# Kernel optimization log

Measured on AMD Instinct MI355X. Metric: run time of the kernel, lower is better.

The kernel has to match this reference:

```python
import jax, jax.numpy as jnp
import numpy as np

B, S, NH, HID, NL = 64, 512, 16, 512, 16
W_WIN, PAD, THR, BW = 5, 2, 5.0, 0.1
D_IN = 1 + 2 * NH


def setup_inputs():
    key = jax.random.key(0)
    ks = jax.random.split(key, 16)
    time = jax.random.uniform(ks[0], (B, S)) * 1000.0
    mag = 15.0 + jax.random.normal(ks[1], (B, S))
    err = 0.01 + 0.1 * jax.random.uniform(ks[2], (B, S))
    sc = 0.05
    p = {}
    p["light_curve"] = jnp.stack([time, mag, err], axis=1)  # (B,3,S)
    p["valid_mask"] = jnp.ones((B, S), dtype=bool)
    p["frequency"] = 0.5 + 4.5 * jax.random.uniform(ks[3], (B,))
    p["W_ih0"] = sc * jax.random.normal(ks[4], (3 * HID, D_IN))
    p["b_ih0"] = jnp.zeros((3 * HID,))
    p["W_hh0"] = sc * jax.random.normal(ks[5], (3 * HID, HID))
    p["b_hh0"] = jnp.zeros((3 * HID,))
    p["W_ih1"] = sc * jax.random.normal(ks[6], (3 * HID, HID))
    p["b_ih1"] = jnp.zeros((3 * HID,))
    p["W_hh1"] = sc * jax.random.normal(ks[7], (3 * HID, HID))
    p["b_hh1"] = jnp.zeros((3 * HID,))
    p["Wl1"] = sc * jax.random.normal(ks[8], (HID, HID))
    p["bl1"] = jnp.zeros((HID,))
    p["Wl2"] = sc * jax.random.normal(ks[9], (NL, HID))
    p["bl2"] = jnp.zeros((NL,))
    return p


def _flag_outliers(phase, mag):
    # Sorted-window weighted (Epanechnikov in circular phase-delta) mean/std outlier test.
    # Caller guarantees all points valid (setup uses an all-True mask), so index_select == identity.
    perm = jnp.argsort(phase)
    ps, ms = phase[perm], mag[perm]

    def windows(x):
        xp = jnp.concatenate([x[-PAD:], x, x[:PAD]])  # circular pad
        return jnp.stack([xp[i:i + S] for i in range(W_WIN)], axis=-1)  # (S, w)

    wp, wm = windows(ps), windows(ms)
    cols = jnp.array([i for i in range(W_WIN) if i != PAD])
    dphi = wp[:, cols] - wp[:, PAD:PAD + 1]
    dphi = jnp.remainder(dphi - 0.5, 1.0) - 0.5
    wgt = 0.75 * (1.0 - dphi ** 2)
    wmm = wm[:, cols]
    wsum = wgt.sum(-1)
    loc = (wmm * wgt).sum(-1) / wsum
    scale = jnp.sqrt((((wmm - loc[:, None]) ** 2) * wgt).sum(-1) / (wsum - 1.0))
    thr = loc + THR * scale
    sigma = jnp.zeros_like(mag).at[perm].set(thr)  # inverse-permute (index_copy_)
    return mag > sigma


def _gru_layer(x, W_ih, b_ih, W_hh, b_hh):
    # torch nn.GRU cell math; x: (B,S,D) -> (B,S,H)
    xW = jnp.einsum('bsd,gd->bsg', x, W_ih) + b_ih  # (B,S,3H)

    def step(h, xt):
        hW = h @ W_hh.T + b_hh
        xr, xz, xn = jnp.split(xt, 3, axis=-1)
        hr, hz, hn = jnp.split(hW, 3, axis=-1)
        r = jax.nn.sigmoid(xr + hr)
        z = jax.nn.sigmoid(xz + hz)
        n = jnp.tanh(xn + r * hn)
        h = (1.0 - z) * n + z * h
        return h, h

    h0 = jnp.zeros((x.shape[0], W_hh.shape[1]), x.dtype)
    _, hs = jax.lax.scan(step, h0, jnp.swapaxes(xW, 0, 1))
    return jnp.swapaxes(hs, 0, 1)


def reference(light_curve, valid_mask, frequency, W_ih0, b_ih0, W_hh0, b_hh0,
              W_ih1, b_ih1, W_hh1, b_hh1, Wl1, bl1, Wl2, bl2):
    time, mag, err = light_curve[:, 0], light_curve[:, 1], light_curve[:, 2]
    period = 2.0 / frequency[:, None]  # fold_with_double_period=True (default)
    phase = jnp.remainder(time, period) / period
    outlier = jax.vmap(_flag_outliers)(phase, mag)
    is_valid = valid_mask & ~outlier

    # periodic-kernel interpolation on 50-point grid; align phase to brightness max
    grid = jnp.linspace(0.0, 1.0, 50)
    delta = grid[None, :, None] - phase[:, None, :]  # (B,50,S)
    K = jnp.exp((jnp.cos(2.0 * jnp.pi * delta) - 1.0) / BW ** 2)
    Wk = is_valid[:, None, :].astype(K.dtype) * K
    Wk = Wk / Wk.sum(-1, keepdims=True)
    smooth = (Wk * mag[:, None, :]).sum(-1)  # (B,50)
    phase = phase - grid[jnp.argmax(smooth, axis=-1)][:, None]

    # sort by phase, invalid points last; scaler=None -> loc 0, scale 1
    big = jnp.finfo(jnp.float32).max
    idx = jnp.argsort(jnp.where(is_valid, phase, big), axis=-1)
    phase = jnp.take_along_axis(phase, idx, -1)
    mag = jnp.take_along_axis(mag, idx, -1)
    is_valid = jnp.take_along_axis(is_valid, idx, -1)

    # Fourier phase embedding [cos_1..cos_H, sin_1..sin_H] + mag -> (B,S,2H+1)
    k = jnp.arange(1, NH + 1, dtype=phase.dtype)
    ang = 2.0 * jnp.pi * phase[:, :, None] * k
    emb = jnp.concatenate([jnp.cos(ang), jnp.sin(ang), mag[:, :, None]], axis=-1)

    ht = _gru_layer(emb, W_ih0, b_ih0, W_hh0, b_hh0)
    ht = _gru_layer(ht, W_ih1, b_ih1, W_hh1, b_hh1)

    m = is_valid[:, :, None].astype(ht.dtype)  # context='average'
    ctx = (ht * m).sum(1) / m.sum(1)
    h1 = jax.nn.gelu(ctx @ Wl1.T + bl1, approximate=False)
    z = h1 @ Wl2.T + bl2
    return z
```

## Files before the change

kernel.cpp:

```cpp
#include <hip/hip_runtime.h>


typedef unsigned short u16;
typedef unsigned int u32;
typedef unsigned long long u64;

__device__ __forceinline__ float b2f(u16 u) { return __uint_as_float(((u32)u) << 16); }
__device__ __forceinline__ float blo(u32 u) { return __uint_as_float(u << 16); }
__device__ __forceinline__ float bhi(u32 u) { return __uint_as_float(u & 0xffff0000u); }
__device__ __forceinline__ u16 f2b(float f) {
    u32 x = __float_as_uint(f);
    u32 r = x + 0x7fffu + ((x >> 16) & 1u);
    return (u16)(r >> 16);
}

#define SS 512
#define TWO_PI 6.28318530717958647692f
#define BIGF 3.402823466e+38f
#define PANEL_ELEMS (1536 * 512)
#define FLAGS_BYTES 32768
#define FL(g, f) (((g) * 16 + (f)) * 16)
#define F_A 0
#define F_B 2
#define F_C 4
#define G_A 6
#define G_B 8
#define G_C 10
#define F_PRE 12
#define F_CTX 14

struct P {
    const void* lc;
    const void* freq;
    const void* W[12];
    void* out;
    void* ws;
    unsigned long long ws_size;
};

__device__ __forceinline__ bool inputs_are_bf16(const void* freq) {
    const u16* q = (const u16*)freq;
    bool ok = true;
    for (int i = 0; i < 64; ++i) {
        float v = b2f(q[i]);
        ok = ok && (v >= 0.4f) && (v <= 5.5f);
    }
    return ok;
}

template<bool BF>
__device__ __forceinline__ float ldw(const void* p, size_t i) {
    if constexpr (BF) return b2f(((const u16*)p)[i]);
    else              return ((const float*)p)[i];
}
template<bool BF>
__device__ __forceinline__ const void* rowp(const void* base, int row) {
    if constexpr (BF) return (const void*)((const u16*)base + (size_t)row * 512);
    else              return (const void*)((const float*)base + (size_t)row * 512);
}

__device__ __forceinline__ void sc_store_f(float* ptr, float v) {
    __hip_atomic_store(ptr, v, __ATOMIC_RELAXED, __HIP_MEMORY_SCOPE_AGENT);
}
__device__ __forceinline__ float sc_load_f(const float* ptr) {
    return __hip_atomic_load(ptr, __ATOMIC_RELAXED, __HIP_MEMORY_SCOPE_AGENT);
}
__device__ __forceinline__ void sc_store_i(int* ptr, int v) {
    __hip_atomic_store(ptr, v, __ATOMIC_RELAXED, __HIP_MEMORY_SCOPE_AGENT);
}
__device__ __forceinline__ int sc_load_i(const int* ptr) {
    return __hip_atomic_load(ptr, __ATOMIC_RELAXED, __HIP_MEMORY_SCOPE_AGENT);
}
__device__ __forceinline__ void waitge(const int* f, int v, int* dead) {
    if (*dead) return;
    int it = 0;
    while (sc_load_i(f) < v) {
        __builtin_amdgcn_s_sleep(1);
        if (++it > 400000) { *dead = 1; break; }
    }
}

template<bool BF>
__device__ void build_panel_one(const void* W, int tid, char* panbase) {
    if constexpr (BF) {
        const uint4* Ws = (const uint4*)W;
        uint4* panel = (uint4*)panbase;
        for (int i = tid; i < 1536 * 64; i += 512) {
            int r = i >> 6, k8 = i & 63;
            panel[(size_t)k8 * 1536 + r] = Ws[i];
        }
    } else {
        const float4* Ws = (const float4*)W;
        float4* panel = (float4*)panbase;
        for (int i = tid; i < 1536 * 128; i += 512) {
            int r = i >> 7, k4 = i & 127;
            panel[(size_t)k4 * 1536 + r] = Ws[i];
        }
    }
}
template<bool BF>
__device__ void build_piece(const void* W, int half, int tid, char* panbase) {
    if constexpr (BF) {
        const uint4* Ws = (const uint4*)W;
        uint4* panel = (uint4*)panbase;
        for (int i = tid; i < 768 * 64; i += 512) {
            int r768 = i >> 6, k8 = i & 63;
            int g3 = r768 >> 8, r = r768 & 255;
            int srcrow = g3 * 512 + half * 256 + r;
            panel[(size_t)k8 * 768 + r768] = Ws[(size_t)srcrow * 64 + k8];
        }
    } else {
        const float4* Ws = (const float4*)W;
        float4* panel = (float4*)panbase;
        for (int i = tid; i < 768 * 128; i += 512) {
            int r768 = i >> 7, k4 = i & 127;
            int g3 = r768 >> 8, r = r768 & 255;
            int srcrow = g3 * 512 + half * 256 + r;
            panel[(size_t)k4 * 768 + r768] = Ws[(size_t)srcrow * 128 + k4];
        }
    }
}

template<bool BF>
__device__ __forceinline__ void tridot_panel(const void* panel, int j,
                                             const float* __restrict__ sh,
                                             float& ar, float& az, float& an) {
    if constexpr (BF) {
        const uint4* pr = (const uint4*)panel + j;
        const uint4* pz = pr + 512;
        const uint4* pn = pr + 1024;
        for (int k0 = 0; k0 < 512; k0 += 8) {
            size_t o = (size_t)(k0 >> 3) * 1536;
            float4 h0 = *(const float4*)&sh[k0];
            float4 h1 = *(const float4*)&sh[k0 + 4];
            uint4 a = pr[o], c = pz[o], d = pn[o];
            ar += blo(a.x) * h0.x + bhi(a.x) * h0.y + blo(a.y) * h0.z + bhi(a.y) * h0.w
                + blo(a.z) * h1.x + bhi(a.z) * h1.y + blo(a.w) * h1.z + bhi(a.w) * h1.w;
            az += blo(c.x) * h0.x + bhi(c.x) * h0.y + blo(c.y) * h0.z + bhi(c.y) * h0.w
                + blo(c.z) * h1.x + bhi(c.z) * h1.y + blo(c.w) * h1.z + bhi(c.w) * h1.w;
            an += blo(d.x) * h0.x + bhi(d.x) * h0.y + blo(d.y) * h0.z + bhi(d.y) * h0.w
                + blo(d.z) * h1.x + bhi(d.z) * h1.y + blo(d.w) * h1.z + bhi(d.w) * h1.w;
        }
    } else {
        const float4* pr = (const float4*)panel + j;
        const float4* pz = pr + 512;
        const float4* pn = pr + 1024;
        for (int k0 = 0; k0 < 512; k0 += 8) {
            size_t o = (size_t)(k0 >> 2) * 1536;
            float4 h0 = *(const float4*)&sh[k0];
            float4 h1 = *(const float4*)&sh[k0 + 4];
            float4 a0 = pr[o], a1 = pr[o + 1536];
            float4 c0 = pz[o], c1 = pz[o + 1536];
            float4 d0 = pn[o], d1 = pn[o + 1536];
            ar += a0.x * h0.x + a0.y * h0.y + a0.z * h0.z + a0.w * h0.w
                + a1.x * h1.x + a1.y * h1.y + a1.z * h1.z + a1.w * h1.w;
            az += c0.x * h0.x + c0.y * h0.y + c0.z * h0.z + c0.w * h0.w
                + c1.x * h1.x + c1.y * h1.y + c1.z * h1.z + c1.w * h1.w;
            an += d0.x * h0.x + d0.y * h0.y + d0.z * h0.z + d0.w * h0.w
                + d1.x * h1.x + d1.y * h1.y + d1.z * h1.z + d1.w * h1.w;
        }
    }
}

template<bool BF>
__device__ __forceinline__ void tridot2(const void* panel, int r, int kh,
                                        const float* __restrict__ ha,
                                        const float* __restrict__ hb,
                                        float& a0r, float& a0z, float& a0n,
                                        float& a1r, float& a1z, float& a1n) {
    const int kbeg = kh * 256;
    if constexpr (BF) {
        const uint4* pr = (const uint4*)panel + r;
        const uint4* pz = pr + 256;
        const uint4* pn = pr + 512;
        for (int k0 = kbeg; k0 < kbeg + 256; k0 += 8) {
            size_t o = (size_t)(k0 >> 3) * 768;
            float4 ha0 = *(const float4*)&ha[k0];
            float4 ha1 = *(const float4*)&ha[k0 + 4];
            float4 hb0 = *(const float4*)&hb[k0];
            float4 hb1 = *(const float4*)&hb[k0 + 4];
            uint4 a = pr[o], c = pz[o], d = pn[o];
            a0r += blo(a.x)*ha0.x + bhi(a.x)*ha0.y + blo(a.y)*ha0.z + bhi(a.y)*ha0.w
                 + blo(a.z)*ha1.x + bhi(a.z)*ha1.y + blo(a.w)*ha1.z + bhi(a.w)*ha1.w;
            a1r += blo(a.x)*hb0.x + bhi(a.x)*hb0.y + blo(a.y)*hb0.z + bhi(a.y)*hb0.w
                 + blo(a.z)*hb1.x + bhi(a.z)*hb1.y + blo(a.w)*hb1.z + bhi(a.w)*hb1.w;
            a0z += blo(c.x)*ha0.x + bhi(c.x)*ha0.y + blo(c.y)*ha0.z + bhi(c.y)*ha0.w
                 + blo(c.z)*ha1.x + bhi(c.z)*ha1.y + blo(c.w)*ha1.z + bhi(c.w)*ha1.w;
            a1z += blo(c.x)*hb0.x + bhi(c.x)*hb0.y + blo(c.y)*hb0.z + bhi(c.y)*hb0.w
                 + blo(c.z)*hb1.x + bhi(c.z)*hb1.y + blo(c.w)*hb1.z + bhi(c.w)*hb1.w;
            a0n += blo(d.x)*ha0.x + bhi(d.x)*ha0.y + blo(d.y)*ha0.z + bhi(d.y)*ha0.w
                 + blo(d.z)*ha1.x + bhi(d.z)*ha1.y + blo(d.w)*ha1.z + bhi(d.w)*ha1.w;
            a1n += blo(d.x)*hb0.x + bhi(d.x)*hb0.y + blo(d.y)*hb0.z + bhi(d.y)*hb0.w
                 + blo(d.z)*hb1.x + bhi(d.z)*hb1.y + blo(d.w)*hb1.z + bhi(d.w)*hb1.w;
        }
    } else {
        const float4* pr = (const float4*)panel + r;
        const float4* pz = pr + 256;
        const float4* pn = pr + 512;
        for (int k0 = kbeg; k0 < kbeg + 256; k0 += 8) {
            size_t o = (size_t)(k0 >> 2) * 768;
            float4 ha0 = *(const float4*)&ha[k0];
            float4 ha1 = *(const float4*)&ha[k0 + 4];
            float4 hb0 = *(const float4*)&hb[k0];
            float4 hb1 = *(const float4*)&hb[k0 + 4];
            float4 a0 = pr[o], a1 = pr[o + 768];
            float4 c0 = pz[o], c1 = pz[o + 768];
            float4 d0 = pn[o], d1 = pn[o + 768];
            a0r += a0.x*ha0.x + a0.y*ha0.y + a0.z*ha0.z + a0.w*ha0.w
                 + a1.x*ha1.x + a1.y*ha1.y + a1.z*ha1.z + a1.w*ha1.w;
            a1r += a0.x*hb0.x + a0.y*hb0.y + a0.z*hb0.z + a0.w*hb0.w
                 + a1.x*hb1.x + a1.y*hb1.y + a1.z*hb1.z + a1.w*hb1.w;
            a0z += c0.x*ha0.x + c0.y*ha0.y + c0.z*ha0.z + c0.w*ha0.w
                 + c1.x*ha1.x + c1.y*ha1.y + c1.z*ha1.z + c1.w*ha1.w;
            a1z += c0.x*hb0.x + c0.y*hb0.y + c0.z*hb0.z + c0.w*hb0.w
                 + c1.x*hb1.x + c1.y*hb1.y + c1.z*hb1.z + c1.w*hb1.w;
            a0n += d0.x*ha0.x + d0.y*ha0.y + d0.z*ha0.z + d0.w*ha0.w
                 + d1.x*ha1.x + d1.y*ha1.y + d1.z*ha1.z + d1.w*ha1.w;
            a1n += d0.x*hb0.x + d0.y*hb0.y + d0.z*hb0.z + d0.w*hb0.w
                 + d1.x*hb1.x + d1.y*hb1.y + d1.z*hb1.z + d1.w*hb1.w;
        }
    }
}

template<bool BF>
__device__ __forceinline__ float dot512(const void* vr, const float* __restrict__ sh) {
    float acc = 0.f;
    if constexpr (BF) {
        const u32* pr = (const u32*)vr;
        for (int k0 = 0; k0 < 512; k0 += 8) {
            float4 h0 = *(const float4*)&sh[k0];
            float4 h1 = *(const float4*)&sh[k0 + 4];
            uint4 a = *(const uint4*)(pr + (k0 >> 1));
            acc += blo(a.x) * h0.x + bhi(a.x) * h0.y + blo(a.y) * h0.z + bhi(a.y) * h0.w
                 + blo(a.z) * h1.x + bhi(a.z) * h1.y + blo(a.w) * h1.z + bhi(a.w) * h1.w;
        }
    } else {
        const float* pr = (const float*)vr;
        for (int k0 = 0; k0 < 512; k0 += 8) {
            float4 h0 = *(const float4*)&sh[k0];
            float4 h1 = *(const float4*)&sh[k0 + 4];
            float4 a0 = *(const float4*)(pr + k0), a1 = *(const float4*)(pr + k0 + 4);
            acc += a0.x * h0.x + a0.y * h0.y + a0.z * h0.z + a0.w * h0.w
                 + a1.x * h1.x + a1.y * h1.y + a1.z * h1.z + a1.w * h1.w;
        }
    }
    return acc;
}

struct PreShm {
    float ph[512], mg[512], skey[512], sig[512], vld[512];
    int   sidx[512];
    float ps2[512], ms2[512], vs2[512];
    float pn[50][8], pd[50][8], smoothv[50];
    float gshift, nv;
};

__device__ void bitonic512(float* skey, int* sidx, int tid) {
    for (int k = 2; k <= 512; k <<= 1) {
        for (int j = k >> 1; j > 0; j >>= 1) {
            int ixj = tid ^ j;
            if (ixj > tid) {
                float ka = skey[tid], kb = skey[ixj];
                int ia = sidx[tid], ib = sidx[ixj];
                bool up = ((tid & k) == 0);
                bool agtb = (ka > kb) || (ka == kb && ia > ib);
                if (agtb == up) {
                    skey[tid] = kb; skey[ixj] = ka;
                    sidx[tid] = ib; sidx[ixj] = ia;
                }
            }
            __syncthreads();
        }
    }
}

template<bool BF>
__device__ void preproc_core(const P& p, PreShm& s, int b, int tid) {
    float period = 2.0f / ldw<BF>(p.freq, b);
    float t = ldw<BF>(p.lc, (size_t)b * 3 * SS + tid);
    float m = ldw<BF>(p.lc, (size_t)b * 3 * SS + SS + tid);
    float ph0 = fmodf(t, period) / period;
    s.ph[tid] = ph0; s.mg[tid] = m;
    s.skey[tid] = ph0; s.sidx[tid] = tid;
    __syncthreads();
    bitonic512(s.skey, s.sidx, tid);
    {
        float pc = s.skey[tid];
        float wv[4], mv[4];
        float wsum = 0.f, wm = 0.f;
        const int offs[4] = {-2, -1, 1, 2};
#pragma unroll
        for (int c = 0; c < 4; ++c) {
            int jj = (tid + offs[c]) & 511;
            float d = s.skey[jj] - pc;
            float u = d - 0.5f; u = u - floorf(u);
            float dphi = u - 0.5f;
            float w = 0.75f * (1.0f - dphi * dphi);
            float mm = s.mg[s.sidx[jj]];
            wv[c] = w; mv[c] = mm;
            wsum += w; wm += w * mm;
        }
        float loc = wm / wsum;
        float s2 = 0.f;
#pragma unroll
        for (int c = 0; c < 4; ++c) { float dm = mv[c] - loc; s2 += dm * dm * wv[c]; }
        float scale = sqrtf(s2 / (wsum - 1.0f));
        s.sig[s.sidx[tid]] = loc + 5.0f * scale;
    }
    __syncthreads();
    s.vld[tid] = (s.mg[tid] > s.sig[tid]) ? 0.0f : 1.0f;
    __syncthreads();
    if (tid == 0) {
        float acc = 0.f;
        for (int i = 0; i < 512; ++i) acc += s.vld[i];
        s.nv = acc;
    }
    {
        int g = tid >> 3, pq = tid & 7;
        if (g < 50) {
            float gv = (float)g * (1.0f / 49.0f);
            float num = 0.f, den = 0.f;
            int s0 = pq * 64;
            for (int ss = s0; ss < s0 + 64; ++ss) {
                float d = gv - s.ph[ss];
                float c = cosf(TWO_PI * d);
                float K = expf((c - 1.0f) * 100.0f);
                float w = s.vld[ss] * K;
                den += w; num += w * s.mg[ss];
            }
            s.pn[g][pq] = num; s.pd[g][pq] = den;
        }
    }
    __syncthreads();
    if (tid < 50) {
        float num = 0.f, den = 0.f;
#pragma unroll
        for (int c = 0; c < 8; ++c) { num += s.pn[tid][c]; den += s.pd[tid][c]; }
        s.smoothv[tid] = num / den;
    }
    __syncthreads();
    if (tid == 0) {
        float best = s.smoothv[0]; int bi = 0;
        for (int g = 1; g < 50; ++g) if (s.smoothv[g] > best) { best = s.smoothv[g]; bi = g; }
        s.gshift = (float)bi * (1.0f / 49.0f);
    }
    __syncthreads();
    float p2 = s.ph[tid] - s.gshift;
    s.ph[tid] = p2;
    s.skey[tid] = (s.vld[tid] > 0.f) ? p2 : BIGF;
    s.sidx[tid] = tid;
    __syncthreads();
    bitonic512(s.skey, s.sidx, tid);
    {
        int o = s.sidx[tid];
        s.ps2[tid] = s.ph[o]; s.ms2[tid] = s.mg[o]; s.vs2[tid] = s.vld[o];
    }
    __syncthreads();
}

struct ShmA {
    PreShm pre;
    float psb[2][512], msb[2][512];
    float h0L[1024];
    float eL[2][34];
    float part[6][256];
    float xp[3][256];
};
struct ShmB { float h0loc[1024]; float part[6][256]; };
struct ShmC {
    float h1L[1024]; float vs2L[2][512]; float nvL[2];
    float ctxL[512], gL[512]; float part[6][256];
};
struct ShmOldA { PreShm pre; float h0[512], h1[512], eL[34]; };
struct ShmU {
    union { ShmA a; ShmB b; ShmC c; ShmOldA o; } u;
    int dead;
};

template<bool BF, bool PAN>
__device__ void run_all(const P& p, ShmU& S) {
    PreShm& pre = S.u.o.pre;
    float* h0 = S.u.o.h0;
    float* h1 = S.u.o.h1;
    float* eL = S.u.o.eL;
    int b = blockIdx.x, tid = threadIdx.x;
    char* panbase = (char*)p.ws + FLAGS_BYTES;
    const size_t PMAT = (size_t)PANEL_ELEMS * (BF ? 2 : 4);

    if constexpr (PAN) {
        build_panel_one<BF>(p.W[2], tid, panbase);
        build_panel_one<BF>(p.W[4], tid, panbase + PMAT);
        build_panel_one<BF>(p.W[6], tid, panbase + 2 * PMAT);
        __threadfence();
    }
    preproc_core<BF>(p, pre, b, tid);

    int j = tid;
    float wr0[33], wz0[33], wn0[33];
#pragma unroll
    for (int d = 0; d < 33; ++d) {
        wr0[d] = ldw<BF>(p.W[0], (size_t)j * 33 + d);
        wz0[d] = ldw<BF>(p.W[0], ((size_t)j + 512) * 33 + d);
        wn0[d] = ldw<BF>(p.W[0], ((size_t)j + 1024) * 33 + d);
    }
    float bi0r = ldw<BF>(p.W[1], j), bi0z = ldw<BF>(p.W[1], j + 512), bi0n = ldw<BF>(p.W[1], j + 1024);
    float bh0r = ldw<BF>(p.W[3], j), bh0z = ldw<BF>(p.W[3], j + 512), bh0n = ldw<BF>(p.W[3], j + 1024);
    float bi1r = ldw<BF>(p.W[5], j), bi1z = ldw<BF>(p.W[5], j + 512), bi1n = ldw<BF>(p.W[5], j + 1024);
    float bh1r = ldw<BF>(p.W[7], j), bh1z = ldw<BF>(p.W[7], j + 512), bh1n = ldw<BF>(p.W[7], j + 1024);

    const void* pan0  = (const void*)panbase;
    const void* pan1x = (const void*)(panbase + PMAT);
    const void* pan1h = (const void*)(panbase + 2 * PMAT);
    const void *w0r = rowp<BF>(p.W[2], j), *w0z = rowp<BF>(p.W[2], j + 512), *w0n = rowp<BF>(p.W[2], j + 1024);
    const void *x1r = rowp<BF>(p.W[4], j), *x1z = rowp<BF>(p.W[4], j + 512), *x1n = rowp<BF>(p.W[4], j + 1024);
    const void *w1r = rowp<BF>(p.W[6], j), *w1z = rowp<BF>(p.W[6], j + 512), *w1n = rowp<BF>(p.W[6], j + 1024);

    h0[j] = 0.f; h1[j] = 0.f;
    float cacc = 0.f;
    __syncthreads();

    for (int tt = 0; tt < 512; ++tt) {
        if (j < 16) {
            float ang = TWO_PI * pre.ps2[tt] * (float)(j + 1);
            float sv, cv; sincosf(ang, &sv, &cv);
            eL[j] = cv; eL[16 + j] = sv;
        }
        if (j == 32) eL[32] = pre.ms2[tt];
        __syncthreads();
        float xr = bi0r, xz = bi0z, xn = bi0n;
#pragma unroll
        for (int d = 0; d < 33; ++d) {
            float e = eL[d];
            xr += wr0[d] * e; xz += wz0[d] * e; xn += wn0[d] * e;
        }
        float ar = bh0r, az = bh0z, an = bh0n;
        if constexpr (PAN) tridot_panel<BF>(pan0, j, h0, ar, az, an);
        else {
            for (int k = 0; k < 512; ++k) {
                float h = h0[k];
                ar += ldw<BF>(w0r, k) * h; az += ldw<BF>(w0z, k) * h; an += ldw<BF>(w0n, k) * h;
            }
        }
        float h0prev = h0[j];
        float r0 = 1.0f / (1.0f + expf(-(xr + ar)));
        float z0 = 1.0f / (1.0f + expf(-(xz + az)));
        float n0 = tanhf(xn + r0 * an);
        float nh0 = (1.0f - z0) * n0 + z0 * h0prev;
        __syncthreads();
        h0[j] = nh0;
        __syncthreads();
        float yr = bi1r, yz = bi1z, yn = bi1n;
        float cr = bh1r, cz = bh1z, cn = bh1n;
        if constexpr (PAN) {
            tridot_panel<BF>(pan1x, j, h0, yr, yz, yn);
            tridot_panel<BF>(pan1h, j, h1, cr, cz, cn);
        } else {
            for (int k = 0; k < 512; ++k) {
                float h = h0[k], g = h1[k];
                yr += ldw<BF>(x1r, k) * h; yz += ldw<BF>(x1z, k) * h; yn += ldw<BF>(x1n, k) * h;
                cr += ldw<BF>(w1r, k) * g; cz += ldw<BF>(w1z, k) * g; cn += ldw<BF>(w1n, k) * g;
            }
        }
        float h1prev = h1[j];
        float r1 = 1.0f / (1.0f + expf(-(yr + cr)));
        float z1 = 1.0f / (1.0f + expf(-(yz + cz)));
        float n1 = tanhf(yn + r1 * cn);
        float nh1 = (1.0f - z1) * n1 + z1 * h1prev;
        cacc += pre.vs2[tt] * nh1;
        __syncthreads();
        h1[j] = nh1;
    }
    __syncthreads();

    h0[j] = cacc / pre.nv;
    __syncthreads();
    float a1 = ldw<BF>(p.W[9], j) + dot512<BF>(rowp<BF>(p.W[8], j), h0);
    float g = 0.5f * a1 * (1.0f + erff(a1 * 0.70710678118654752440f));
    __syncthreads();
    h1[j] = g;
    __syncthreads();
    if (j < 16) {
        float a2 = ldw<BF>(p.W[11], j) + dot512<BF>(rowp<BF>(p.W[10], j), h1);
        if constexpr (BF) ((u16*)p.out)[(size_t)b * 16 + j] = f2b(a2);
        else              ((float*)p.out)[(size_t)b * 16 + j] = a2;
    }
}

__global__ __launch_bounds__(512) void fused_kernel_old(P p) {
    __shared__ ShmU S;
    bool bf = inputs_are_bf16(p.freq);
    u64 PMAT = bf ? 1572864ull : 3145728ull;
    bool pan = (p.ws && p.ws_size >= (u64)FLAGS_BYTES + 3 * PMAT);
    if (bf) { if (pan) run_all<true, true>(p, S);  else run_all<true, false>(p, S); }
    else    { if (pan) run_all<false, true>(p, S); else run_all<false, false>(p, S); }
}


template<bool BF>
__device__ void runA(const P& p, ShmU& S, int g, int hf, int tid, char* pan,
                     float* h0r, float* pp, int* flags) {
    int* dead = &S.dead;
    build_piece<BF>(p.W[2], hf, tid, pan);
    __threadfence();
    int myb = 2 * g + hf, ob = 2 * g + (1 - hf);
    preproc_core<BF>(p, S.u.a.pre, myb, tid);
    sc_store_f(&pp[(size_t)myb * 2048 + tid], S.u.a.pre.ps2[tid]);
    sc_store_f(&pp[(size_t)myb * 2048 + 512 + tid], S.u.a.pre.ms2[tid]);
    sc_store_f(&pp[(size_t)myb * 2048 + 1024 + tid], S.u.a.pre.vs2[tid]);
    if (tid == 0) sc_store_f(&pp[(size_t)myb * 2048 + 1536], S.u.a.pre.nv);
    asm volatile("s_waitcnt vmcnt(0)" ::: "memory");
    __syncthreads();
    if (tid == 0) sc_store_i(&flags[FL(g, F_PRE + hf)], 1);
    S.u.a.psb[hf][tid] = S.u.a.pre.ps2[tid];
    S.u.a.msb[hf][tid] = S.u.a.pre.ms2[tid];
    if (tid == 0) waitge(&flags[FL(g, F_PRE + (1 - hf))], 1, dead);
    __syncthreads();
    S.u.a.psb[1 - hf][tid] = sc_load_f(&pp[(size_t)ob * 2048 + tid]);
    S.u.a.msb[1 - hf][tid] = sc_load_f(&pp[(size_t)ob * 2048 + 512 + tid]);

    const int r = tid & 255, kh = tid >> 8;
    const int j = hf * 256 + r;
    const float bi0r = ldw<BF>(p.W[1], j), bi0z = ldw<BF>(p.W[1], j + 512), bi0n = ldw<BF>(p.W[1], j + 1024);
    const float bh0r = ldw<BF>(p.W[3], j), bh0z = ldw<BF>(p.W[3], j + 512), bh0n = ldw<BF>(p.W[3], j + 1024);

    float* h0L = S.u.a.h0L;
    h0L[tid] = 0.f; h0L[tid + 512] = 0.f;
    __syncthreads();

    for (int t = 0; t < 512; ++t) {
        if (t > 0) {
            if (tid == 0) waitge(&flags[FL(g, F_A + (1 - hf))], t, dead);
            __syncthreads();
            h0L[kh * 512 + (1 - hf) * 256 + r] =
                sc_load_f(&h0r[(size_t)g * 2048 + ((t - 1) & 1) * 1024 + (1 - hf) * 512 + kh * 256 + r]);
            __syncthreads();
            if (tid == 0) sc_store_i(&flags[FL(g, G_A + hf)], t);
        }
        if (tid < 16) {
            float ang = TWO_PI * S.u.a.psb[0][t] * (float)(tid + 1);
            float sv, cv; sincosf(ang, &sv, &cv);
            S.u.a.eL[0][tid] = cv; S.u.a.eL[0][16 + tid] = sv;
        } else if (tid < 32) {
            int k = tid - 16;
            float ang = TWO_PI * S.u.a.psb[1][t] * (float)(k + 1);
            float sv, cv; sincosf(ang, &sv, &cv);
            S.u.a.eL[1][k] = cv; S.u.a.eL[1][16 + k] = sv;
        }
        if (tid == 32) S.u.a.eL[0][32] = S.u.a.msb[0][t];
        if (tid == 33) S.u.a.eL[1][32] = S.u.a.msb[1][t];
        __syncthreads();

        float xr = bi0r, xz = bi0z, xn = bi0n;
#pragma unroll
        for (int d = 0; d < 33; ++d) {
            float e = S.u.a.eL[kh][d];
            xr += ldw<BF>(p.W[0], (size_t)j * 33 + d) * e;
            xz += ldw<BF>(p.W[0], ((size_t)j + 512) * 33 + d) * e;
            xn += ldw<BF>(p.W[0], ((size_t)j + 1024) * 33 + d) * e;
        }
        float p0r = 0.f, p0z = 0.f, p0n = 0.f, p1r = 0.f, p1z = 0.f, p1n = 0.f;
        tridot2<BF>(pan, r, kh, &h0L[0], &h0L[512], p0r, p0z, p0n, p1r, p1z, p1n);
        if (kh == 1) {
            S.u.a.part[0][r] = p0r; S.u.a.part[1][r] = p0z; S.u.a.part[2][r] = p0n;
            S.u.a.part[3][r] = p1r; S.u.a.part[4][r] = p1z; S.u.a.part[5][r] = p1n;
            S.u.a.xp[0][r] = xr; S.u.a.xp[1][r] = xz; S.u.a.xp[2][r] = xn;
        }
        __syncthreads();
        float nh00 = 0.f, nh01 = 0.f;
        if (kh == 0) {
            float ar0 = bh0r + p0r + S.u.a.part[0][r];
            float az0 = bh0z + p0z + S.u.a.part[1][r];
            float an0 = bh0n + p0n + S.u.a.part[2][r];
            float ar1 = bh0r + p1r + S.u.a.part[3][r];
            float az1 = bh0z + p1z + S.u.a.part[4][r];
            float an1 = bh0n + p1n + S.u.a.part[5][r];
            float x1r = S.u.a.xp[0][r], x1z = S.u.a.xp[1][r], x1n = S.u.a.xp[2][r];
            float h0p0 = h0L[j], h0p1 = h0L[512 + j];
            float r0 = 1.f / (1.f + expf(-(xr + ar0)));
            float z0 = 1.f / (1.f + expf(-(xz + az0)));
            float n0 = tanhf(xn + r0 * an0);
            nh00 = (1.f - z0) * n0 + z0 * h0p0;
            float r1 = 1.f / (1.f + expf(-(x1r + ar1)));
            float z1 = 1.f / (1.f + expf(-(x1z + az1)));
            float n1 = tanhf(x1n + r1 * an1);
            nh01 = (1.f - z1) * n1 + z1 * h0p1;
            h0L[j] = nh00; h0L[512 + j] = nh01;
        }
        if (t >= 2) {
            if (tid == 0) waitge(&flags[FL(g, G_A + (1 - hf))], t - 1, dead);
            if (tid == 1) waitge(&flags[FL(g, G_B + 0)], t - 1, dead);
            if (tid == 2) waitge(&flags[FL(g, G_B + 1)], t - 1, dead);
        }
        __syncthreads();
        if (kh == 0) {
            float* dst = &h0r[(size_t)g * 2048 + (t & 1) * 1024 + hf * 512];
            sc_store_f(&dst[r], nh00);
            sc_store_f(&dst[256 + r], nh01);
        }
        asm volatile("s_waitcnt vmcnt(0)" ::: "memory");
        __syncthreads();
        if (tid == 0) sc_store_i(&flags[FL(g, F_A + hf)], t + 1);
    }
}

template<bool BF>
__device__ void runB(const P& p, ShmU& S, int g, int hf, int tid, char* pan,
                     float* h0r, float* yrng, int* flags) {
    int* dead = &S.dead;
    build_piece<BF>(p.W[4], hf, tid, pan);
    __threadfence();
    __syncthreads();
    const int r = tid & 255, kh = tid >> 8;
    const int j = hf * 256 + r;
    const float bi1r = ldw<BF>(p.W[5], j), bi1z = ldw<BF>(p.W[5], j + 512), bi1n = ldw<BF>(p.W[5], j + 1024);
    float* h0loc = S.u.b.h0loc;

    for (int t = 0; t < 512; ++t) {
        if (tid == 0) waitge(&flags[FL(g, F_A + 0)], t + 1, dead);
        if (tid == 1) waitge(&flags[FL(g, F_A + 1)], t + 1, dead);
        __syncthreads();
        const float* src = &h0r[(size_t)g * 2048 + (t & 1) * 1024];
        h0loc[kh * 512 + r]       = sc_load_f(&src[0 * 512 + kh * 256 + r]);
        h0loc[kh * 512 + 256 + r] = sc_load_f(&src[1 * 512 + kh * 256 + r]);
        __syncthreads();
        if (tid == 0) sc_store_i(&flags[FL(g, G_B + hf)], t + 1);
        float p0r = 0.f, p0z = 0.f, p0n = 0.f, p1r = 0.f, p1z = 0.f, p1n = 0.f;
        tridot2<BF>(pan, r, kh, &h0loc[0], &h0loc[512], p0r, p0z, p0n, p1r, p1z, p1n);
        if (kh == 1) {
            S.u.b.part[0][r] = p0r; S.u.b.part[1][r] = p0z; S.u.b.part[2][r] = p0n;
            S.u.b.part[3][r] = p1r; S.u.b.part[4][r] = p1z; S.u.b.part[5][r] = p1n;
        }
        if (tid == 0 && t >= 2) waitge(&flags[FL(g, G_C + hf)], t - 1, dead);
        __syncthreads();
        if (kh == 0) {
            float y0r = bi1r + p0r + S.u.b.part[0][r];
            float y0z = bi1z + p0z + S.u.b.part[1][r];
            float y0n = bi1n + p0n + S.u.b.part[2][r];
            float y1r = bi1r + p1r + S.u.b.part[3][r];
            float y1z = bi1z + p1z + S.u.b.part[4][r];
            float y1n = bi1n + p1n + S.u.b.part[5][r];
            float* slot = &yrng[(size_t)g * 6144 + (t & 1) * 3072 + hf * 1536];
            sc_store_f(&slot[r], y0r);         sc_store_f(&slot[256 + r], y1r);
            sc_store_f(&slot[512 + r], y0z);   sc_store_f(&slot[768 + r], y1z);
            sc_store_f(&slot[1024 + r], y0n);  sc_store_f(&slot[1280 + r], y1n);
        }
        asm volatile("s_waitcnt vmcnt(0)" ::: "memory");
        __syncthreads();
        if (tid == 0) sc_store_i(&flags[FL(g, F_B + hf)], t + 1);
    }
}

template<bool BF>
__device__ void runC(const P& p, ShmU& S, int g, int hf, int tid, char* pan,
                     float* yrng, float* h1r, float* pp, float* ctxb, int* flags) {
    int* dead = &S.dead;
    build_piece<BF>(p.W[6], hf, tid, pan);
    __threadfence();
    if (tid == 0) waitge(&flags[FL(g, F_PRE + 0)], 1, dead);
    if (tid == 1) waitge(&flags[FL(g, F_PRE + 1)], 1, dead);
    __syncthreads();
    S.u.c.vs2L[0][tid] = sc_load_f(&pp[(size_t)(2 * g) * 2048 + 1024 + tid]);
    S.u.c.vs2L[1][tid] = sc_load_f(&pp[(size_t)(2 * g + 1) * 2048 + 1024 + tid]);
    if (tid == 0) {
        S.u.c.nvL[0] = sc_load_f(&pp[(size_t)(2 * g) * 2048 + 1536]);
        S.u.c.nvL[1] = sc_load_f(&pp[(size_t)(2 * g + 1) * 2048 + 1536]);
    }
    float* h1L = S.u.c.h1L;
    h1L[tid] = 0.f; h1L[tid + 512] = 0.f;
    __syncthreads();

    const int r = tid & 255, kh = tid >> 8;
    const int j = hf * 256 + r;
    const float bh1r = ldw<BF>(p.W[7], j), bh1z = ldw<BF>(p.W[7], j + 512), bh1n = ldw<BF>(p.W[7], j + 1024);
    float cacc0 = 0.f, cacc1 = 0.f;

    for (int t = 0; t < 512; ++t) {
        if (tid == 0) waitge(&flags[FL(g, F_B + hf)], t + 1, dead);
        if (t > 0 && tid == 1) waitge(&flags[FL(g, F_C + (1 - hf))], t, dead);
        __syncthreads();
        if (t > 0) {
            h1L[kh * 512 + (1 - hf) * 256 + r] =
                sc_load_f(&h1r[(size_t)g * 2048 + ((t - 1) & 1) * 1024 + (1 - hf) * 512 + kh * 256 + r]);
        }
        float y0r = 0.f, y0z = 0.f, y0n = 0.f, y1r = 0.f, y1z = 0.f, y1n = 0.f;
        if (kh == 0) {
            const float* slot = &yrng[(size_t)g * 6144 + (t & 1) * 3072 + hf * 1536];
            y0r = sc_load_f(&slot[r]);         y1r = sc_load_f(&slot[256 + r]);
            y0z = sc_load_f(&slot[512 + r]);   y1z = sc_load_f(&slot[768 + r]);
            y0n = sc_load_f(&slot[1024 + r]);  y1n = sc_load_f(&slot[1280 + r]);
        }
        __syncthreads();
        if (tid == 0) sc_store_i(&flags[FL(g, G_C + hf)], t + 1);
        float p0r = 0.f, p0z = 0.f, p0n = 0.f, p1r = 0.f, p1z = 0.f, p1n = 0.f;
        tridot2<BF>(pan, r, kh, &h1L[0], &h1L[512], p0r, p0z, p0n, p1r, p1z, p1n);
        if (kh == 1) {
            S.u.c.part[0][r] = p0r; S.u.c.part[1][r] = p0z; S.u.c.part[2][r] = p0n;
            S.u.c.part[3][r] = p1r; S.u.c.part[4][r] = p1z; S.u.c.part[5][r] = p1n;
        }
        __syncthreads();
        float nh10 = 0.f, nh11 = 0.f;
        if (kh == 0) {
            float cr0 = bh1r + p0r + S.u.c.part[0][r];
            float cz0 = bh1z + p0z + S.u.c.part[1][r];
            float cn0 = bh1n + p0n + S.u.c.part[2][r];
            float cr1 = bh1r + p1r + S.u.c.part[3][r];
            float cz1 = bh1z + p1z + S.u.c.part[4][r];
            float cn1 = bh1n + p1n + S.u.c.part[5][r];
            float h1p0 = h1L[j], h1p1 = h1L[512 + j];
            float r0 = 1.f / (1.f + expf(-(y0r + cr0)));
            float z0 = 1.f / (1.f + expf(-(y0z + cz0)));
            float n0 = tanhf(y0n + r0 * cn0);
            nh10 = (1.f - z0) * n0 + z0 * h1p0;
            float r1 = 1.f / (1.f + expf(-(y1r + cr1)));
            float z1 = 1.f / (1.f + expf(-(y1z + cz1)));
            float n1 = tanhf(y1n + r1 * cn1);
            nh11 = (1.f - z1) * n1 + z1 * h1p1;
            cacc0 += S.u.c.vs2L[0][t] * nh10;
            cacc1 += S.u.c.vs2L[1][t] * nh11;
            h1L[j] = nh10; h1L[512 + j] = nh11;
        }
        if (t >= 2 && tid == 2) waitge(&flags[FL(g, G_C + (1 - hf))], t, dead);
        __syncthreads();
        if (kh == 0) {
            float* dst = &h1r[(size_t)g * 2048 + (t & 1) * 1024 + hf * 512];
            sc_store_f(&dst[r], nh10);
            sc_store_f(&dst[256 + r], nh11);
        }
        asm volatile("s_waitcnt vmcnt(0)" ::: "memory");
        __syncthreads();
        if (tid == 0) sc_store_i(&flags[FL(g, F_C + hf)], t + 1);
    }

    if (kh == 0) {
        sc_store_f(&ctxb[(size_t)g * 1024 + hf * 512 + r], cacc0);
        sc_store_f(&ctxb[(size_t)g * 1024 + hf * 512 + 256 + r], cacc1);
    }
    asm volatile("s_waitcnt vmcnt(0)" ::: "memory");
    __syncthreads();
    if (tid == 0) {
        sc_store_i(&flags[FL(g, F_CTX + hf)], 1);
        waitge(&flags[FL(g, F_CTX + (1 - hf))], 1, dead);
    }
    __syncthreads();
    float nv = S.u.c.nvL[hf];
    S.u.c.ctxL[tid] = sc_load_f(&ctxb[(size_t)g * 1024 + (tid >> 8) * 512 + hf * 256 + (tid & 255)]) / nv;
    __syncthreads();
    float a1 = ldw<BF>(p.W[9], tid) + dot512<BF>(rowp<BF>(p.W[8], tid), S.u.c.ctxL);
    float gg = 0.5f * a1 * (1.0f + erff(a1 * 0.70710678118654752440f));
    __syncthreads();
    S.u.c.gL[tid] = gg;
    __syncthreads();
    if (tid < 16) {
        float a2 = ldw<BF>(p.W[11], tid) + dot512<BF>(rowp<BF>(p.W[10], tid), S.u.c.gL);
        int hb = 2 * g + hf;
        if constexpr (BF) ((u16*)p.out)[(size_t)hb * 16 + tid] = f2b(a2);
        else              ((float*)p.out)[(size_t)hb * 16 + tid] = a2;
    }
}

template<bool BF>
__device__ void run_pipe(const P& p, ShmU& S) {
    const int bid = blockIdx.x;
    const int piece = bid & 7;
    if (piece >= 6) return;
    const int g = bid >> 3;
    const int role = piece >> 1, hf = piece & 1;
    const int tid = threadIdx.x;
    if (tid == 0) S.dead = 0;
    __syncthreads();

    char* wsb = (char*)p.ws;
    int* flags = (int*)wsb;
    const size_t PIECE = BF ? 786432 : 1572864;
    char* pans = wsb + FLAGS_BYTES;
    char* mypan = pans + (size_t)piece * PIECE;
    float* h0r  = (float*)(pans + 6 * PIECE);
    float* yrng = h0r + (size_t)32 * 2048;
    float* h1r  = yrng + (size_t)32 * 6144;
    float* pp   = h1r + (size_t)32 * 2048;
    float* ctxb = pp + (size_t)64 * 2048;

    if (role == 0)      runA<BF>(p, S, g, hf, tid, mypan, h0r, pp, flags);
    else if (role == 1) runB<BF>(p, S, g, hf, tid, mypan, h0r, yrng, flags);
    else                runC<BF>(p, S, g, hf, tid, mypan, yrng, h1r, pp, ctxb, flags);
}

__global__ __launch_bounds__(512) void fused_kernel_pipe(P p) {
    __shared__ ShmU S;
    if (inputs_are_bf16(p.freq)) run_pipe<true>(p, S);
    else                         run_pipe<false>(p, S);
}

extern "C" void kernel_launch(void* const* d_in, const int* in_sizes, int n_in,
                              void* d_out, int out_size, void* d_ws, size_t ws_size,
                              hipStream_t stream) {
    P p;
    p.lc = d_in[0];
    p.freq = d_in[2];
    for (int i = 0; i < 12; ++i) p.W[i] = d_in[3 + i];
    p.out = d_out;
    p.ws = d_ws;
    p.ws_size = (unsigned long long)ws_size;

    const size_t need_pipe = 11436032ull;
    if (d_ws && ws_size >= need_pipe) {
        hipMemsetAsync(d_ws, 0, FLAGS_BYTES, stream);
        fused_kernel_pipe<<<256, 512, 0, stream>>>(p);
    } else {
        fused_kernel_old<<<64, 512, 0, stream>>>(p);
    }
    (void)in_sizes; (void)n_in; (void)out_size;
}
```

Before: 12.44 ms.

## Overlap cross-block waits with compute and relayout W_ih0 for coalesced reads

In stage A, each block copies its half of W_ih0 into a transposed per-block workspace buffer so the input-projection loop reads coalesced fp32 values. The wait on the sibling's hidden state is moved after the embedding computation, and its load is issued before the projection loop so the latency overlaps that work. In stage C, the wait on stage B's y values is deferred until after the recurrent matvec, which takes it off the critical path. The change needs more workspace (the launch threshold is raised) and reorders the flag signalling, which adds some risk of synchronisation mistakes between blocks.

```diff
diff --git a/kernel.cpp b/kernel.cpp
--- a/kernel.cpp
+++ b/kernel.cpp
@@ -498,9 +498,15 @@
 
 template<bool BF>
 __device__ void runA(const P& p, ShmU& S, int g, int hf, int tid, char* pan,
-                     float* h0r, float* pp, int* flags) {
+                     float* h0r, float* pp, float* w0p, int* flags) {
     int* dead = &S.dead;
     build_piece<BF>(p.W[2], hf, tid, pan);
+    float* w0m = w0p + (size_t)hf * 25344;
+    for (int i = tid; i < 33 * 768; i += 512) {
+        int d = i / 768, rr = i - d * 768;
+        int g3 = rr >> 8, r2 = rr & 255;
+        w0m[i] = ldw<BF>(p.W[0], (size_t)(g3 * 512 + hf * 256 + r2) * 33 + d);
+    }
     __threadfence();
     int myb = 2 * g + hf, ob = 2 * g + (1 - hf);
     preproc_core<BF>(p, S.u.a.pre, myb, tid);
@@ -528,14 +534,6 @@
     __syncthreads();
 
     for (int t = 0; t < 512; ++t) {
-        if (t > 0) {
-            if (tid == 0) waitge(&flags[FL(g, F_A + (1 - hf))], t, dead);
-            __syncthreads();
-            h0L[kh * 512 + (1 - hf) * 256 + r] =
-                sc_load_f(&h0r[(size_t)g * 2048 + ((t - 1) & 1) * 1024 + (1 - hf) * 512 + kh * 256 + r]);
-            __syncthreads();
-            if (tid == 0) sc_store_i(&flags[FL(g, G_A + hf)], t);
-        }
         if (tid < 16) {
             float ang = TWO_PI * S.u.a.psb[0][t] * (float)(tid + 1);
             float sv, cv; sincosf(ang, &sv, &cv);
@@ -548,16 +546,25 @@
         }
         if (tid == 32) S.u.a.eL[0][32] = S.u.a.msb[0][t];
         if (tid == 33) S.u.a.eL[1][32] = S.u.a.msb[1][t];
-        __syncthreads();
-
+        if (t > 0 && tid == 0) waitge(&flags[FL(g, F_A + (1 - hf))], t, dead);
+        __syncthreads();
+
+        float sib = 0.f;
+        if (t > 0)
+            sib = sc_load_f(&h0r[(size_t)g * 2048 + ((t - 1) & 1) * 1024 + (1 - hf) * 512 + kh * 256 + r]);
         float xr = bi0r, xz = bi0z, xn = bi0n;
 #pragma unroll
         for (int d = 0; d < 33; ++d) {
             float e = S.u.a.eL[kh][d];
-            xr += ldw<BF>(p.W[0], (size_t)j * 33 + d) * e;
-            xz += ldw<BF>(p.W[0], ((size_t)j + 512) * 33 + d) * e;
-            xn += ldw<BF>(p.W[0], ((size_t)j + 1024) * 33 + d) * e;
-        }
+            int o = d * 768 + r;
+            xr += w0m[o] * e;
+            xz += w0m[o + 256] * e;
+            xn += w0m[o + 512] * e;
+        }
+        if (t > 0) h0L[kh * 512 + (1 - hf) * 256 + r] = sib;
+        __syncthreads();
+        if (t > 0 && tid == 0) sc_store_i(&flags[FL(g, G_A + hf)], t);
+
         float p0r = 0.f, p0z = 0.f, p0n = 0.f, p1r = 0.f, p1z = 0.f, p1n = 0.f;
         tridot2<BF>(pan, r, kh, &h0L[0], &h0L[512], p0r, p0z, p0n, p1r, p1z, p1n);
         if (kh == 1) {
@@ -675,31 +682,29 @@
     float cacc0 = 0.f, cacc1 = 0.f;
 
     for (int t = 0; t < 512; ++t) {
-        if (tid == 0) waitge(&flags[FL(g, F_B + hf)], t + 1, dead);
         if (t > 0 && tid == 1) waitge(&flags[FL(g, F_C + (1 - hf))], t, dead);
         __syncthreads();
         if (t > 0) {
             h1L[kh * 512 + (1 - hf) * 256 + r] =
                 sc_load_f(&h1r[(size_t)g * 2048 + ((t - 1) & 1) * 1024 + (1 - hf) * 512 + kh * 256 + r]);
         }
-        float y0r = 0.f, y0z = 0.f, y0n = 0.f, y1r = 0.f, y1z = 0.f, y1n = 0.f;
-        if (kh == 0) {
-            const float* slot = &yrng[(size_t)g * 6144 + (t & 1) * 3072 + hf * 1536];
-            y0r = sc_load_f(&slot[r]);         y1r = sc_load_f(&slot[256 + r]);
-            y0z = sc_load_f(&slot[512 + r]);   y1z = sc_load_f(&slot[768 + r]);
-            y0n = sc_load_f(&slot[1024 + r]);  y1n = sc_load_f(&slot[1280 + r]);
-        }
-        __syncthreads();
-        if (tid == 0) sc_store_i(&flags[FL(g, G_C + hf)], t + 1);
+        __syncthreads();
+
         float p0r = 0.f, p0z = 0.f, p0n = 0.f, p1r = 0.f, p1z = 0.f, p1n = 0.f;
         tridot2<BF>(pan, r, kh, &h1L[0], &h1L[512], p0r, p0z, p0n, p1r, p1z, p1n);
         if (kh == 1) {
             S.u.c.part[0][r] = p0r; S.u.c.part[1][r] = p0z; S.u.c.part[2][r] = p0n;
             S.u.c.part[3][r] = p1r; S.u.c.part[4][r] = p1z; S.u.c.part[5][r] = p1n;
         }
-        __syncthreads();
+        if (tid == 0) waitge(&flags[FL(g, F_B + hf)], t + 1, dead);
+        __syncthreads();
+
         float nh10 = 0.f, nh11 = 0.f;
         if (kh == 0) {
+            const float* slot = &yrng[(size_t)g * 6144 + (t & 1) * 3072 + hf * 1536];
+            float y0r = sc_load_f(&slot[r]);         float y1r = sc_load_f(&slot[256 + r]);
+            float y0z = sc_load_f(&slot[512 + r]);   float y1z = sc_load_f(&slot[768 + r]);
+            float y0n = sc_load_f(&slot[1024 + r]);  float y1n = sc_load_f(&slot[1280 + r]);
             float cr0 = bh1r + p0r + S.u.c.part[0][r];
             float cz0 = bh1z + p0z + S.u.c.part[1][r];
             float cn0 = bh1n + p0n + S.u.c.part[2][r];
@@ -717,8 +722,10 @@
             nh11 = (1.f - z1) * n1 + z1 * h1p1;
             cacc0 += S.u.c.vs2L[0][t] * nh10;
             cacc1 += S.u.c.vs2L[1][t] * nh11;
-            h1L[j] = nh10; h1L[512 + j] = nh11;
-        }
+        }
+        __syncthreads();
+        if (tid == 0) sc_store_i(&flags[FL(g, G_C + hf)], t + 1);
+        if (kh == 0) { h1L[j] = nh10; h1L[512 + j] = nh11; }
         if (t >= 2 && tid == 2) waitge(&flags[FL(g, G_C + (1 - hf))], t, dead);
         __syncthreads();
         if (kh == 0) {
@@ -779,8 +786,9 @@
     float* h1r  = yrng + (size_t)32 * 6144;
     float* pp   = h1r + (size_t)32 * 2048;
     float* ctxb = pp + (size_t)64 * 2048;
-
-    if (role == 0)      runA<BF>(p, S, g, hf, tid, mypan, h0r, pp, flags);
+    float* w0p  = ctxb + (size_t)32 * 1024;
+
+    if (role == 0)      runA<BF>(p, S, g, hf, tid, mypan, h0r, pp, w0p, flags);
     else if (role == 1) runB<BF>(p, S, g, hf, tid, mypan, h0r, yrng, flags);
     else                runC<BF>(p, S, g, hf, tid, mypan, yrng, h1r, pp, ctxb, flags);
 }
@@ -802,7 +810,7 @@
     p.ws = d_ws;
     p.ws_size = (unsigned long long)ws_size;
 
-    const size_t need_pipe = 11436032ull;
+    const size_t need_pipe = 11638784ull;
     if (d_ws && ws_size >= need_pipe) {
         hipMemsetAsync(d_ws, 0, FLAGS_BYTES, stream);
         fused_kernel_pipe<<<256, 512, 0, stream>>>(p);
```

Result: slower. 24.86 ms (+99.9%).
